# Kernel tuning notes

Measured on AMD Instinct MI355X. Metric: run time of the kernel, lower is better.

The kernel has to match this reference:

```python
import jax, jax.numpy as jnp
import numpy as np

QUERY_SIZE = 1024
MEMORY_SIZE = 1024
ATTN_SIZE = 512
B, T = 64, 2048


def setup_inputs() -> dict:
    key = jax.random.key(0)
    k1, k2, k3, k4, k5 = jax.random.split(key, 5)
    query = jax.random.normal(k1, (B, QUERY_SIZE), dtype=jnp.float32)
    memory = jax.random.normal(k2, (B, T, MEMORY_SIZE), dtype=jnp.float32)
    # nn.Linear weights: shape (out_features, in_features); y = x @ W.T
    s_q = 1.0 / np.sqrt(QUERY_SIZE)
    s_m = 1.0 / np.sqrt(MEMORY_SIZE)
    s_v = 1.0 / np.sqrt(ATTN_SIZE)
    W_query = jax.random.uniform(k3, (ATTN_SIZE, QUERY_SIZE), jnp.float32, -s_q, s_q)
    W_memory = jax.random.uniform(k4, (ATTN_SIZE, MEMORY_SIZE), jnp.float32, -s_m, s_m)
    W_v = jax.random.uniform(k5, (1, ATTN_SIZE), jnp.float32, -s_v, s_v)
    return {"query": query, "memory": memory, "W_query": W_query,
            "W_memory": W_memory, "W_v": W_v}


def reference(query, memory, W_query, W_memory, W_v):
    # w_query: [B, A]; w_memory: [B, T, A]
    w_query = query @ W_query.T
    w_memory = jnp.einsum("btm,am->bta", memory, W_memory)
    # additive score: v^T tanh(wq + wm) -> [B, T]
    scores = jnp.einsum("bta,a->bt", jnp.tanh(w_query[:, None, :] + w_memory), W_v[0])
    alpha = jax.nn.softmax(scores, axis=-1)  # [B, T]
    # context = alpha @ memory -> [B, 1, M]
    context = jnp.einsum("bt,btm->bm", alpha, memory)[:, None, :]
    return (alpha, context)
```

## Files before the change

kernel.cpp:

```cpp
#include <hip/hip_runtime.h>
#include <hip/hip_bf16.h>
#include <cstdint>
#include <cstddef>

#define Bn 64
#define Tn 2048
#define Mn 1024
#define An 512
#define Qn 1024

#define RT 64
#define BK 32
#define NKC (Mn / BK)

typedef __attribute__((ext_vector_type(8))) short short8;
typedef __attribute__((ext_vector_type(4))) float f32x4;
typedef __attribute__((ext_vector_type(2))) float f32x2;
typedef __attribute__((ext_vector_type(4))) unsigned short us4;

static __device__ __forceinline__ unsigned short f2bf(float f) {
  uint32_t u = __float_as_uint(f);
  u += 0x7fff + ((u >> 16) & 1);
  return (unsigned short)(u >> 16);
}

static __device__ __forceinline__ void gl_lds16(const void* g, void* l) {
  __builtin_amdgcn_global_load_lds(
      (const __attribute__((address_space(1))) unsigned int*)g,
      (__attribute__((address_space(3))) unsigned int*)l, 16, 0, 0);
}

__global__ void zero_kernel(float* __restrict__ ctx, float* __restrict__ Zacc) {
  int i = blockIdx.x * 256 + threadIdx.x;
  if (i < Bn * Mn) ctx[i] = 0.0f;
  else if (i < Bn * Mn + Bn) Zacc[i - Bn * Mn] = 0.0f;
}

__global__ void cvt_wm_kernel(const float* __restrict__ Wm, unsigned short* __restrict__ out) {
  int i = blockIdx.x * 256 + threadIdx.x;
  if (i < An * Mn) out[i] = f2bf(Wm[i]);
}

__global__ void wq_kernel(const float* __restrict__ query, const float* __restrict__ Wq,
                          float* __restrict__ wqout) {
  __shared__ __align__(16) float qs[Qn];
  const int b = blockIdx.x >> 2;
  const int ag = blockIdx.x & 3;
  const int tid = threadIdx.x;
  for (int i = tid; i < Qn; i += 128) qs[i] = query[b * Qn + i];
  __syncthreads();
  const int a = ag * 128 + tid;
  const f32x4* w = (const f32x4*)(Wq + (size_t)a * Qn);
  const f32x4* q4 = (const f32x4*)qs;
  float acc = 0.f;
#pragma unroll 8
  for (int m = 0; m < Qn / 4; ++m) {
    f32x4 wv = w[m];
    f32x4 qv = q4[m];
    acc += wv.x * qv.x + wv.y * qv.y + wv.z * qv.z + wv.w * qv.w;
  }
  wqout[b * An + a] = acc;
}

__launch_bounds__(512, 4)
__global__ void fused_kernel(const float* __restrict__ mem,
                             const float* __restrict__ wq,
                             const unsigned short* __restrict__ Wmb,
                             const float* __restrict__ Wv,
                             float* __restrict__ out,
                             float* __restrict__ Zacc) {
  __shared__ __align__(16) unsigned short As[2][RT * BK];
  __shared__ __align__(16) unsigned short Bs[2][An * BK];
  __shared__ float s_score[RT];
  __shared__ float s_e[RT];

  const int tid = threadIdx.x;
  const int b  = blockIdx.x & (Bn - 1);
  const int tt = blockIdx.x >> 6;
  const int t0 = tt * RT;

  const int lane = tid & 63;
  const int w = tid >> 6;
  const int l15 = lane & 15;
  const int quad = lane >> 4;

  if (tid < RT) s_score[tid] = 0.f;

  const int arow = tid >> 3;
  const int ah = tid & 7;
  const float* asrc = mem + ((size_t)(b * Tn + t0 + arow)) * Mn + ah * 4;
  const int au = ((ah >> 1) + (arow >> 1)) & 3;
  const int aoff = arow * BK + au * 8 + (ah & 1) * 4;

  const int ba0 = w * 64 + (lane >> 2);
  const int bj = lane & 3;

  int aro[4], bro[4];
#pragma unroll
  for (int rt = 0; rt < 4; ++rt) {
    int row = rt * 16 + l15;
    aro[rt] = row * BK + (((quad + (row >> 1)) & 3) * 8);
  }
#pragma unroll
  for (int ct = 0; ct < 4; ++ct) {
    int a = w * 64 + ct * 16 + l15;
    bro[ct] = a * BK + (((quad + (a >> 1)) & 3) * 8);
  }

  f32x4 av = *(const f32x4*)asrc;
  {
    us4 o; o.x = f2bf(av.x); o.y = f2bf(av.y); o.z = f2bf(av.z); o.w = f2bf(av.w);
    *(us4*)&As[0][aoff] = o;
  }
#pragma unroll
  for (int i = 0; i < 4; ++i) {
    int a = ba0 + i * 16;
    int q = (bj - (a >> 1)) & 3;
    gl_lds16(Wmb + (size_t)a * Mn + q * 8, &Bs[0][(size_t)(w * 4 + i) * 512]);
  }
  __syncthreads();

  f32x4 acc[4][4] = {};

  for (int kc = 0; kc < NKC; ++kc) {
    const int p = kc & 1, np = p ^ 1;
    if (kc + 1 < NKC) {
      av = *(const f32x4*)(asrc + (kc + 1) * BK);
#pragma unroll
      for (int i = 0; i < 4; ++i) {
        int a = ba0 + i * 16;
        int q = (bj - (a >> 1)) & 3;
        gl_lds16(Wmb + (size_t)a * Mn + (kc + 1) * BK + q * 8,
                 &Bs[np][(size_t)(w * 4 + i) * 512]);
      }
    }

    short8 af[4], bf[4];
#pragma unroll
    for (int i = 0; i < 4; ++i) af[i] = *(const short8*)&As[p][aro[i]];
#pragma unroll
    for (int i = 0; i < 4; ++i) bf[i] = *(const short8*)&Bs[p][bro[i]];

#pragma unroll
    for (int rt = 0; rt < 4; ++rt)
#pragma unroll
      for (int ct = 0; ct < 4; ++ct)
        acc[rt][ct] = __builtin_amdgcn_mfma_f32_16x16x32_bf16(af[rt], bf[ct], acc[rt][ct], 0, 0, 0);

    if (kc + 1 < NKC) {
      us4 o; o.x = f2bf(av.x); o.y = f2bf(av.y); o.z = f2bf(av.z); o.w = f2bf(av.w);
      *(us4*)&As[np][aoff] = o;
    }
    __syncthreads();
  }

  const float* wqb = wq + b * An;
  {
    float rs[4][4];
#pragma unroll
    for (int rt = 0; rt < 4; ++rt)
#pragma unroll
      for (int g = 0; g < 4; ++g) rs[rt][g] = 0.f;

#pragma unroll
    for (int ct = 0; ct < 4; ++ct) {
      const int a = w * 64 + ct * 16 + l15;
      const float wqa = wqb[a];
      const float va = Wv[a];
#pragma unroll
      for (int rt = 0; rt < 4; ++rt) {
#pragma unroll
        for (int g = 0; g < 4; ++g) {
          float x = wqa + acc[rt][ct][g];
          float ez = __expf(2.0f * x);
          float th = 1.0f - 2.0f * __builtin_amdgcn_rcpf(ez + 1.0f);
          rs[rt][g] += va * th;
        }
      }
    }
#pragma unroll
    for (int rt = 0; rt < 4; ++rt) {
#pragma unroll
      for (int g = 0; g < 4; ++g) {
        float v = rs[rt][g];
        v += __shfl_xor(v, 1);
        v += __shfl_xor(v, 2);
        v += __shfl_xor(v, 4);
        v += __shfl_xor(v, 8);
        if (l15 == 0) atomicAdd(&s_score[rt * 16 + quad * 4 + g], v);
      }
    }
  }
  __syncthreads();

  if (tid < RT) {
    float e = __expf(s_score[tid]);
    s_e[tid] = e;
    out[(size_t)b * Tn + t0 + tid] = e;
    float z = e;
    z += __shfl_xor(z, 1);
    z += __shfl_xor(z, 2);
    z += __shfl_xor(z, 4);
    z += __shfl_xor(z, 8);
    z += __shfl_xor(z, 16);
    z += __shfl_xor(z, 32);
    if (lane == 0) atomicAdd(&Zacc[b], z);
  }
  __syncthreads();

  {
    const float* mrow = mem + ((size_t)(b * Tn + t0)) * Mn + 2 * tid;
    float c0 = 0.f, c1 = 0.f;
#pragma unroll 8
    for (int r = 0; r < RT; ++r) {
      f32x2 v = *(const f32x2*)(mrow + (size_t)r * Mn);
      float e = s_e[r];
      c0 += e * v.x;
      c1 += e * v.y;
    }
    float* ctx = out + Bn * Tn + (size_t)b * Mn + 2 * tid;
    atomicAdd(&ctx[0], c0);
    atomicAdd(&ctx[1], c1);
  }
}

__global__ void finalize_kernel(float* __restrict__ out, const float* __restrict__ Zacc) {
  int i = blockIdx.x * 256 + threadIdx.x;
  if (i < Bn * Tn) {
    int b = i >> 11;
    out[i] /= Zacc[b];
  } else if (i < Bn * Tn + Bn * Mn) {
    int j = i - Bn * Tn;
    int b = j >> 10;
    out[i] /= Zacc[b];
  }
}

extern "C" void kernel_launch(void* const* d_in, const int* in_sizes, int n_in,
                              void* d_out, int out_size, void* d_ws, size_t ws_size,
                              hipStream_t stream) {
  const float* query    = (const float*)d_in[0];
  const float* memory   = (const float*)d_in[1];
  const float* W_query  = (const float*)d_in[2];
  const float* W_memory = (const float*)d_in[3];
  const float* W_v      = (const float*)d_in[4];
  float* out = (float*)d_out;

  float* wq = (float*)d_ws;
  unsigned short* Wmb = (unsigned short*)((char*)d_ws + (size_t)Bn * An * 4);
  float* Zacc = (float*)((char*)d_ws + (size_t)Bn * An * 4 + (size_t)An * Mn * 2);

  zero_kernel<<<(Bn * Mn + Bn + 255) / 256, 256, 0, stream>>>(out + Bn * Tn, Zacc);
  cvt_wm_kernel<<<(An * Mn + 255) / 256, 256, 0, stream>>>(W_memory, Wmb);
  wq_kernel<<<Bn * 4, 128, 0, stream>>>(query, W_query, wq);
  fused_kernel<<<Bn * (Tn / RT), 512, 0, stream>>>(memory, wq, Wmb, W_v, out, Zacc);
  finalize_kernel<<<(Bn * Tn + Bn * Mn + 255) / 256, 256, 0, stream>>>(out, Zacc);
}
```

Before: 898.4 us.

## Load W_memory fragments directly to registers, widen A staging, replace context atomics with partials

The bf16 W_memory tile is no longer staged through LDS via global_load_lds. Each wave now loads its B fragments straight from global (L2-resident) into double-buffered registers. The memory tile is staged in larger 128-wide K groups with a 16-way XOR swizzle, so there are four MFMA steps per barrier instead of one. Per-tile context sums are written to a workspace partials buffer and reduced in a new finalize kernel rather than with global float atomics. This trades LDS traffic and barriers for more global/L2 loads and extra workspace memory, and falls back to atomics if the workspace is too small.

```diff
diff --git a/kernel.cpp b/kernel.cpp
--- a/kernel.cpp
+++ b/kernel.cpp
@@ -10,8 +10,9 @@
 #define Qn 1024
 
 #define RT 64
-#define BK 32
-#define NKC (Mn / BK)
+#define GK 128
+#define NG 8
+#define NCH 32
 
 typedef __attribute__((ext_vector_type(8))) short short8;
 typedef __attribute__((ext_vector_type(4))) float f32x4;
@@ -22,12 +23,6 @@
   uint32_t u = __float_as_uint(f);
   u += 0x7fff + ((u >> 16) & 1);
   return (unsigned short)(u >> 16);
-}
-
-static __device__ __forceinline__ void gl_lds16(const void* g, void* l) {
-  __builtin_amdgcn_global_load_lds(
-      (const __attribute__((address_space(1))) unsigned int*)g,
-      (__attribute__((address_space(3))) unsigned int*)l, 16, 0, 0);
 }
 
 __global__ void zero_kernel(float* __restrict__ ctx, float* __restrict__ Zacc) {
@@ -68,9 +63,9 @@
                              const unsigned short* __restrict__ Wmb,
                              const float* __restrict__ Wv,
                              float* __restrict__ out,
-                             float* __restrict__ Zacc) {
-  __shared__ __align__(16) unsigned short As[2][RT * BK];
-  __shared__ __align__(16) unsigned short Bs[2][An * BK];
+                             float* __restrict__ Zacc,
+                             float* __restrict__ partials) {
+  __shared__ __align__(16) unsigned short Abuf[2][RT * GK];
   __shared__ float s_score[RT];
   __shared__ float s_e[RT];
 
@@ -89,67 +84,75 @@
   const int arow = tid >> 3;
   const int ah = tid & 7;
   const float* asrc = mem + ((size_t)(b * Tn + t0 + arow)) * Mn + ah * 4;
-  const int au = ((ah >> 1) + (arow >> 1)) & 3;
-  const int aoff = arow * BK + au * 8 + (ah & 1) * 4;
-
-  const int ba0 = w * 64 + (lane >> 2);
-  const int bj = lane & 3;
-
-  int aro[4], bro[4];
-#pragma unroll
-  for (int rt = 0; rt < 4; ++rt) {
-    int row = rt * 16 + l15;
-    aro[rt] = row * BK + (((quad + (row >> 1)) & 3) * 8);
-  }
-#pragma unroll
-  for (int ct = 0; ct < 4; ++ct) {
-    int a = w * 64 + ct * 16 + l15;
-    bro[ct] = a * BK + (((quad + (a >> 1)) & 3) * 8);
-  }
-
-  f32x4 av = *(const f32x4*)asrc;
+  const int w_lu = ah >> 1;
+  const int w_half = (ah & 1) * 4;
+
+  auto awr = [&](unsigned short* buf, int kcl, f32x4 v) {
+    int off = arow * GK + ((((kcl << 2) + w_lu + arow) & 15) << 3) + w_half;
+    us4 o; o.x = f2bf(v.x); o.y = f2bf(v.y); o.z = f2bf(v.z); o.w = f2bf(v.w);
+    *(us4*)&buf[off] = o;
+  };
+
+  const unsigned short* bbase[4];
+#pragma unroll
+  for (int ct = 0; ct < 4; ++ct)
+    bbase[ct] = Wmb + (size_t)(w * 64 + ct * 16 + l15) * Mn + quad * 8;
+
   {
-    us4 o; o.x = f2bf(av.x); o.y = f2bf(av.y); o.z = f2bf(av.z); o.w = f2bf(av.w);
-    *(us4*)&As[0][aoff] = o;
-  }
-#pragma unroll
-  for (int i = 0; i < 4; ++i) {
-    int a = ba0 + i * 16;
-    int q = (bj - (a >> 1)) & 3;
-    gl_lds16(Wmb + (size_t)a * Mn + q * 8, &Bs[0][(size_t)(w * 4 + i) * 512]);
-  }
+    f32x4 v0 = *(const f32x4*)(asrc + 0 * 32);
+    f32x4 v1 = *(const f32x4*)(asrc + 1 * 32);
+    f32x4 v2 = *(const f32x4*)(asrc + 2 * 32);
+    f32x4 v3 = *(const f32x4*)(asrc + 3 * 32);
+    awr((unsigned short*)Abuf[0], 0, v0);
+    awr((unsigned short*)Abuf[0], 1, v1);
+    awr((unsigned short*)Abuf[0], 2, v2);
+    awr((unsigned short*)Abuf[0], 3, v3);
+  }
+  short8 bb[2][4];
+#pragma unroll
+  for (int ct = 0; ct < 4; ++ct) bb[0][ct] = *(const short8*)(bbase[ct]);
   __syncthreads();
 
   f32x4 acc[4][4] = {};
-
-  for (int kc = 0; kc < NKC; ++kc) {
-    const int p = kc & 1, np = p ^ 1;
-    if (kc + 1 < NKC) {
-      av = *(const f32x4*)(asrc + (kc + 1) * BK);
-#pragma unroll
-      for (int i = 0; i < 4; ++i) {
-        int a = ba0 + i * 16;
-        int q = (bj - (a >> 1)) & 3;
-        gl_lds16(Wmb + (size_t)a * Mn + (kc + 1) * BK + q * 8,
-                 &Bs[np][(size_t)(w * 4 + i) * 512]);
-      }
-    }
-
-    short8 af[4], bf[4];
-#pragma unroll
-    for (int i = 0; i < 4; ++i) af[i] = *(const short8*)&As[p][aro[i]];
-#pragma unroll
-    for (int i = 0; i < 4; ++i) bf[i] = *(const short8*)&Bs[p][bro[i]];
-
-#pragma unroll
-    for (int rt = 0; rt < 4; ++rt)
-#pragma unroll
-      for (int ct = 0; ct < 4; ++ct)
-        acc[rt][ct] = __builtin_amdgcn_mfma_f32_16x16x32_bf16(af[rt], bf[ct], acc[rt][ct], 0, 0, 0);
-
-    if (kc + 1 < NKC) {
-      us4 o; o.x = f2bf(av.x); o.y = f2bf(av.y); o.z = f2bf(av.z); o.w = f2bf(av.w);
-      *(us4*)&As[np][aoff] = o;
+  f32x4 ap0, ap1, ap2, ap3;
+
+  for (int g = 0; g < NG; ++g) {
+    const int base = g * 4;
+    unsigned short* nbuf = (unsigned short*)Abuf[(g & 1) ^ 1];
+    const unsigned short* cbuf = (const unsigned short*)Abuf[g & 1];
+#pragma unroll
+    for (int j = 0; j < 4; ++j) {
+      const int kc = base + j;
+      const int cu = j & 1;
+      const int nx = cu ^ 1;
+      if (kc + 1 < NCH) {
+#pragma unroll
+        for (int ct = 0; ct < 4; ++ct)
+          bb[nx][ct] = *(const short8*)(bbase[ct] + (size_t)(kc + 1) * 32);
+      }
+      if (g + 1 < NG) {
+        if (j == 0) { ap0 = *(const f32x4*)(asrc + (size_t)(base + 4) * 32);
+                      ap1 = *(const f32x4*)(asrc + (size_t)(base + 5) * 32); }
+        if (j == 1) { ap2 = *(const f32x4*)(asrc + (size_t)(base + 6) * 32); }
+        if (j == 2) { ap3 = *(const f32x4*)(asrc + (size_t)(base + 7) * 32); }
+      }
+      short8 af[4];
+#pragma unroll
+      for (int rt = 0; rt < 4; ++rt) {
+        int row = rt * 16 + l15;
+        int off = row * GK + ((((j << 2) + quad + row) & 15) << 3);
+        af[rt] = *(const short8*)&cbuf[off];
+      }
+#pragma unroll
+      for (int rt = 0; rt < 4; ++rt)
+#pragma unroll
+        for (int ct = 0; ct < 4; ++ct)
+          acc[rt][ct] = __builtin_amdgcn_mfma_f32_16x16x32_bf16(af[rt], bb[cu][ct], acc[rt][ct], 0, 0, 0);
+      if (g + 1 < NG) {
+        if (j == 1) awr(nbuf, 0, ap0);
+        if (j == 2) awr(nbuf, 1, ap1);
+        if (j == 3) { awr(nbuf, 2, ap2); awr(nbuf, 3, ap3); }
+      }
     }
     __syncthreads();
   }
@@ -160,7 +163,7 @@
 #pragma unroll
     for (int rt = 0; rt < 4; ++rt)
 #pragma unroll
-      for (int g = 0; g < 4; ++g) rs[rt][g] = 0.f;
+      for (int g2 = 0; g2 < 4; ++g2) rs[rt][g2] = 0.f;
 
 #pragma unroll
     for (int ct = 0; ct < 4; ++ct) {
@@ -170,24 +173,24 @@
 #pragma unroll
       for (int rt = 0; rt < 4; ++rt) {
 #pragma unroll
-        for (int g = 0; g < 4; ++g) {
-          float x = wqa + acc[rt][ct][g];
+        for (int g2 = 0; g2 < 4; ++g2) {
+          float x = wqa + acc[rt][ct][g2];
           float ez = __expf(2.0f * x);
           float th = 1.0f - 2.0f * __builtin_amdgcn_rcpf(ez + 1.0f);
-          rs[rt][g] += va * th;
+          rs[rt][g2] += va * th;
         }
       }
     }
 #pragma unroll
     for (int rt = 0; rt < 4; ++rt) {
 #pragma unroll
-      for (int g = 0; g < 4; ++g) {
-        float v = rs[rt][g];
+      for (int g2 = 0; g2 < 4; ++g2) {
+        float v = rs[rt][g2];
         v += __shfl_xor(v, 1);
         v += __shfl_xor(v, 2);
         v += __shfl_xor(v, 4);
         v += __shfl_xor(v, 8);
-        if (l15 == 0) atomicAdd(&s_score[rt * 16 + quad * 4 + g], v);
+        if (l15 == 0) atomicAdd(&s_score[rt * 16 + quad * 4 + g2], v);
       }
     }
   }
@@ -218,21 +221,41 @@
       c0 += e * v.x;
       c1 += e * v.y;
     }
-    float* ctx = out + Bn * Tn + (size_t)b * Mn + 2 * tid;
-    atomicAdd(&ctx[0], c0);
-    atomicAdd(&ctx[1], c1);
+    if (partials) {
+      f32x2 o; o.x = c0; o.y = c1;
+      *(f32x2*)(partials + ((size_t)((b << 5) + tt)) * Mn + 2 * tid) = o;
+    } else {
+      float* ctx = out + Bn * Tn + (size_t)b * Mn + 2 * tid;
+      atomicAdd(&ctx[0], c0);
+      atomicAdd(&ctx[1], c1);
+    }
   }
 }
 
 __global__ void finalize_kernel(float* __restrict__ out, const float* __restrict__ Zacc) {
   int i = blockIdx.x * 256 + threadIdx.x;
   if (i < Bn * Tn) {
-    int b = i >> 11;
-    out[i] /= Zacc[b];
+    out[i] /= Zacc[i >> 11];
   } else if (i < Bn * Tn + Bn * Mn) {
     int j = i - Bn * Tn;
-    int b = j >> 10;
-    out[i] /= Zacc[b];
+    out[i] /= Zacc[j >> 10];
+  }
+}
+
+__global__ void finalize_part_kernel(float* __restrict__ out, const float* __restrict__ Zacc,
+                                     const float* __restrict__ partials) {
+  int i = blockIdx.x * 256 + threadIdx.x;
+  if (i < Bn * Tn) {
+    out[i] /= Zacc[i >> 11];
+  } else if (i < Bn * Tn + Bn * Mn) {
+    int j = i - Bn * Tn;
+    int bb2 = j >> 10;
+    int m = j & (Mn - 1);
+    const float* p = partials + (size_t)(bb2 << 5) * Mn + m;
+    float s = 0.f;
+#pragma unroll
+    for (int t2 = 0; t2 < 32; ++t2) s += p[(size_t)t2 * Mn];
+    out[i] = s / Zacc[bb2];
   }
 }
 
@@ -246,13 +269,21 @@
   const float* W_v      = (const float*)d_in[4];
   float* out = (float*)d_out;
 
+  const size_t off_wm = (size_t)Bn * An * 4;
+  const size_t off_z  = off_wm + (size_t)An * Mn * 2;
+  const size_t off_p  = off_z + 256;
+  const size_t need_p = off_p + (size_t)Bn * 32 * Mn * 4;
   float* wq = (float*)d_ws;
-  unsigned short* Wmb = (unsigned short*)((char*)d_ws + (size_t)Bn * An * 4);
-  float* Zacc = (float*)((char*)d_ws + (size_t)Bn * An * 4 + (size_t)An * Mn * 2);
+  unsigned short* Wmb = (unsigned short*)((char*)d_ws + off_wm);
+  float* Zacc = (float*)((char*)d_ws + off_z);
+  float* partials = (ws_size >= need_p) ? (float*)((char*)d_ws + off_p) : nullptr;
 
   zero_kernel<<<(Bn * Mn + Bn + 255) / 256, 256, 0, stream>>>(out + Bn * Tn, Zacc);
   cvt_wm_kernel<<<(An * Mn + 255) / 256, 256, 0, stream>>>(W_memory, Wmb);
   wq_kernel<<<Bn * 4, 128, 0, stream>>>(query, W_query, wq);
-  fused_kernel<<<Bn * (Tn / RT), 512, 0, stream>>>(memory, wq, Wmb, W_v, out, Zacc);
-  finalize_kernel<<<(Bn * Tn + Bn * Mn + 255) / 256, 256, 0, stream>>>(out, Zacc);
-}
+  fused_kernel<<<Bn * (Tn / RT), 512, 0, stream>>>(memory, wq, Wmb, W_v, out, Zacc, partials);
+  if (partials)
+    finalize_part_kernel<<<(Bn * Tn + Bn * Mn + 255) / 256, 256, 0, stream>>>(out, Zacc, partials);
+  else
+    finalize_kernel<<<(Bn * Tn + Bn * Mn + 255) / 256, 256, 0, stream>>>(out, Zacc);
+}
```

Result: slower. 1.039 ms (+15.7%).
